# Kernel optimization log

Measured on AMD Instinct MI355X. Metric: run time of the kernel, lower is better.

The kernel has to match this reference:

```python
import jax, jax.numpy as jnp
import numpy as np

KH, KW = 3, 3
PAD = (1, 1, 1, 1)  # torch F.pad order: (W_left, W_right, H_top, H_bottom)
STRIDE = 1
B, CIN, COUT, H, W = 4, 32, 32, 128, 128


def setup_inputs() -> dict:
    key = jax.random.key(0)
    k1, k2, k3, k4 = jax.random.split(key, 4)
    f = jax.random.normal(k1, (B, CIN, H, W), jnp.float32)
    # orientation field components (cos/sin of a random angle field)
    theta = jax.random.uniform(k2, (B, CIN, H, W), jnp.float32, 0.0, 2.0 * np.pi)
    r0 = jnp.cos(theta)
    r1 = jnp.sin(theta)
    # learned conv weight (nn.Conv2d default uniform init, no bias)
    fan_in = CIN * KH * KW
    bound = 1.0 / np.sqrt(fan_in)
    w = jax.random.uniform(k3, (COUT, CIN, KH, KW), jnp.float32, -bound, bound)
    # frozen wr: (randn * pi * 100) / a with a = 100  ->  randn * pi
    wr = jax.random.normal(k4, (COUT, CIN, KH, KW), jnp.float32) * np.pi
    return {"f": f, "r0": r0, "r1": r1, "w": w, "wr": wr}


def _rot90(w):
    # torch: w.permute(0,1,2,4,3).flip([4]) on the (kh,kw) dims
    return jnp.flip(jnp.swapaxes(w, -1, -2), -1)


def _conv_single(f, r0, r1, w, wr):
    # f, r0, r1: (B, Cin, Hp, Wp);  w, wr: (Cout, Cin, KH, KW)
    Hp, Wp = f.shape[2], f.shape[3]
    he = Hp - PAD[0] - PAD[1]
    we = Wp - PAD[2] - PAD[3]
    s = STRIDE
    out = None
    for i in range(KH):
        for j in range(KW):
            fw = f[:, :, i:i + he:s, j:j + we:s]    # (B, Cin, h, w)
            r0w = r0[:, :, i:i + he:s, j:j + we:s]
            r1w = r1[:, :, i:i + he:s, j:j + we:s]
            c = jnp.cos(wr[:, :, i, j])[None, :, :, None, None]   # (1, Cout, Cin, 1, 1)
            sn = jnp.sin(wr[:, :, i, j])[None, :, :, None, None]
            # lambda_theta: relu of orientation-projected field, (B, Cout, Cin, h, w)
            lam = jax.nn.relu(c * r0w[:, None] + sn * r1w[:, None])
            term = jnp.einsum('bchw,oc,bochw->bohw', fw, w[:, :, i, j], lam)
            out = term if out is None else out + term
    return out  # (B, Cout, h, w)


def _forward(f, r0, r1, w, wr):
    pl, pr, pt, pb = PAD
    pad = ((0, 0), (0, 0), (pt, pb), (pl, pr))
    fp = jnp.pad(f, pad)
    r0p = jnp.pad(r0, pad)
    r1p = jnp.pad(r1, pad)
    orient = jnp.arange(4, dtype=f.dtype) * jnp.asarray(np.pi / 2, f.dtype)
    outs = []
    wk = w
    for o in range(4):
        if o > 0:
            wk = _rot90(wk)
        outs.append(_conv_single(fp, r0p, r1p, wk, wr + orient[o]))
    stacked = jnp.stack(outs, axis=2)              # (B, Cout, 4, h, w)
    idx = jnp.argmax(stacked, axis=2)              # (B, Cout, h, w)
    out = jnp.take_along_axis(stacked, idx[:, :, None], axis=2)[:, :, 0]
    out_r = orient[idx]                            # winning orientation angle
    return out, jnp.cos(out_r), jnp.sin(out_r)


def reference(f, r0, r1, w, wr):
    return _forward(f, r0, r1, w, wr)
```

## Files before the change

### kernel.cpp

```cpp
#include <hip/hip_runtime.h>


typedef float v2f __attribute__((ext_vector_type(2)));

#define B_    4
#define CIN_  32
#define COUT_ 32
#define H_    128
#define W_    128
#define OUTSZ_ (B_ * COUT_ * H_ * W_)

__global__ __launch_bounds__(256)
void build_wtab(const float* __restrict__ w, const float* __restrict__ wr,
                float* __restrict__ tab)
{
    int idx = blockIdx.x * 256 + threadIdx.x;
    if (idx >= CIN_ * 9 * COUT_) return;
    int oc  = idx & 31;
    int t2  = idx >> 5;
    int tap = t2 % 9;
    int cc  = t2 / 9;
    int i = tap / 3, j = tap - i * 3;
    int base = (oc * CIN_ + cc) * 9;
    float w0 = w[base + i * 3 + j];
    float w1 = w[base + (2 - j) * 3 + i];
    float w2 = w[base + (2 - i) * 3 + (2 - j)];
    float w3 = w[base + j * 3 + (2 - i)];
    float S, C;
    sincosf(wr[base + i * 3 + j], &S, &C);
    float* dst = tab + (size_t)idx * 8;
    dst[0] = C;  dst[1] = S;
    dst[2] = w0; dst[3] = w1;
    dst[4] = w2; dst[5] = w3;
    dst[6] = 0.0f; dst[7] = 0.0f;
}

__global__ __launch_bounds__(512, 4)
void orient_conv_kernel(const float* __restrict__ f,
                        const float* __restrict__ r0,
                        const float* __restrict__ r1,
                        const float* __restrict__ tab,
                        float* __restrict__ out)
{
    __shared__ float sF[612], sR0[612], sR1[612];

    const int tid   = threadIdx.x;
    const int oc    = tid & 31;
    const int pxg   = tid >> 5;
    const int p     = pxg << 1;
    const int bid   = blockIdx.x;
    const int b     = bid >> 8;
    const int rem   = bid & 255;
    const int h     = rem >> 1;
    const int wbase = (rem & 1) << 6;

    int  r_0 = tid / 68, rm0 = tid - r_0 * 68;
    int  c_0 = rm0 >> 1, s_0 = rm0 & 1;
    int  gh0 = h + r_0 - 1, gw0 = wbase + c_0 + (s_0 << 5) - 1;
    bool ok0 = ((unsigned)gh0 < (unsigned)H_) & ((unsigned)gw0 < (unsigned)W_);
    int  go0 = ok0 ? (gh0 * W_ + gw0) : 0;

    int  sl1 = tid + 512;
    bool hv1 = sl1 < 612;
    int  r_1 = sl1 / 68, rm1 = sl1 - r_1 * 68;
    int  c_1 = rm1 >> 1, s_1 = rm1 & 1;
    int  gh1 = h + r_1 - 1, gw1 = wbase + c_1 + (s_1 << 5) - 1;
    bool ok1 = hv1 & ((unsigned)gh1 < (unsigned)H_) & ((unsigned)gw1 < (unsigned)W_);
    int  go1 = ok1 ? (gh1 * W_ + gw1) : 0;

    const int chanBase = b * (CIN_ * H_ * W_);

    v2f acc[2][4];
#pragma unroll
    for (int q = 0; q < 2; ++q)
#pragma unroll
        for (int o = 0; o < 4; ++o) acc[q][o] = (v2f)(0.0f);

    for (int cc = 0; cc < CIN_; ++cc) {
        const int base = chanBase + cc * (H_ * W_);
        sF [tid] = ok0 ? f [base + go0] : 0.0f;
        sR0[tid] = ok0 ? r0[base + go0] : 0.0f;
        sR1[tid] = ok0 ? r1[base + go0] : 0.0f;
        if (hv1) {
            sF [sl1] = ok1 ? f [base + go1] : 0.0f;
            sR0[sl1] = ok1 ? r0[base + go1] : 0.0f;
            sR1[sl1] = ok1 ? r1[base + go1] : 0.0f;
        }
        __syncthreads();

        const float* wcc = tab + (((size_t)cc * 9) << 5) * 8 + oc * 8;

#pragma unroll
        for (int i = 0; i < 3; ++i) {
            const int wi = i * 68 + (p << 1);
            float4 fA  = *reinterpret_cast<const float4*>(&sF [wi]);
            float4 fB  = *reinterpret_cast<const float4*>(&sF [wi + 4]);
            float4 aA  = *reinterpret_cast<const float4*>(&sR0[wi]);
            float4 aB  = *reinterpret_cast<const float4*>(&sR0[wi + 4]);
            float4 bA  = *reinterpret_cast<const float4*>(&sR1[wi]);
            float4 bB  = *reinterpret_cast<const float4*>(&sR1[wi + 4]);
            v2f fP[4]  = {{fA.x, fA.y}, {fA.z, fA.w}, {fB.x, fB.y}, {fB.z, fB.w}};
            v2f r0P[4] = {{aA.x, aA.y}, {aA.z, aA.w}, {aB.x, aB.y}, {aB.z, aB.w}};
            v2f r1P[4] = {{bA.x, bA.y}, {bA.z, bA.w}, {bB.x, bB.y}, {bB.z, bB.w}};
#pragma unroll
            for (int j = 0; j < 3; ++j) {
                const float* wp = wcc + (i * 3 + j) * 256;
                float4 wA = *reinterpret_cast<const float4*>(wp);
                v2f    wB = *reinterpret_cast<const v2f*>(wp + 4);
                v2f Cd  = {wA.x, wA.x}, Sd  = {wA.y, wA.y};
                v2f w0d = {wA.z, wA.z}, w1d = {wA.w, wA.w};
                v2f w2d = {wB.x, wB.x}, w3d = {wB.y, wB.y};
#pragma unroll
                for (int q = 0; q < 2; ++q) {
                    v2f fv  = fP [q + j];
                    v2f r0v = r0P[q + j];
                    v2f r1v = r1P[q + j];
                    v2f u  = __builtin_elementwise_fma(Cd, r0v, Sd * r1v);
                    v2f vv = __builtin_elementwise_fma(Cd, r1v, -(Sd * r0v));
                    v2f g0 = __builtin_elementwise_max(u,  (v2f)(0.0f));
                    v2f g1 = __builtin_elementwise_max(vv, (v2f)(0.0f));
                    v2f g2 = g0 - u;
                    v2f g3 = g1 - vv;
                    acc[q][0] = __builtin_elementwise_fma(fv * g0, w0d, acc[q][0]);
                    acc[q][1] = __builtin_elementwise_fma(fv * g1, w1d, acc[q][1]);
                    acc[q][2] = __builtin_elementwise_fma(fv * g2, w2d, acc[q][2]);
                    acc[q][3] = __builtin_elementwise_fma(fv * g3, w3d, acc[q][3]);
                }
            }
        }
        __syncthreads();
    }

    const float cosv[4] = {1.0f, -4.37113883e-08f, -1.0f, 1.19248806e-08f};
    const float sinv[4] = {0.0f, 1.0f, -8.74227766e-08f, -1.0f};
#pragma unroll
    for (int q = 0; q < 2; ++q) {
#pragma unroll
        for (int k = 0; k < 2; ++k) {
            int wcol = wbase + p + q + (k << 5);
            float a0 = acc[q][0][k], a1 = acc[q][1][k];
            float a2 = acc[q][2][k], a3 = acc[q][3][k];
            float best = a0; int bi = 0;
            if (a1 > best) { best = a1; bi = 1; }
            if (a2 > best) { best = a2; bi = 2; }
            if (a3 > best) { best = a3; bi = 3; }
            size_t o = ((size_t)(b * COUT_ + oc) * H_ + h) * W_ + wcol;
            out[o]              = best;
            out[o + OUTSZ_]     = cosv[bi];
            out[o + 2 * OUTSZ_] = sinv[bi];
        }
    }
}

extern "C" void kernel_launch(void* const* d_in, const int* in_sizes, int n_in,
                              void* d_out, int out_size, void* d_ws, size_t ws_size,
                              hipStream_t stream)
{
    const float* f  = (const float*)d_in[0];
    const float* r0 = (const float*)d_in[1];
    const float* r1 = (const float*)d_in[2];
    const float* w  = (const float*)d_in[3];
    const float* wr = (const float*)d_in[4];
    float* out = (float*)d_out;
    float* tab = (float*)d_ws;

    build_wtab<<<dim3(36), dim3(256), 0, stream>>>(w, wr, tab);
    orient_conv_kernel<<<dim3(B_ * H_ * 2), dim3(512), 0, stream>>>(
        f, r0, r1, tab, out);
}
```

Baseline: 306.1 us.

## Stage eight input channels per barrier with register prefetch and scalar 4-pixel tiles

```diff
diff --git a/kernel.cpp b/kernel.cpp
--- a/kernel.cpp
+++ b/kernel.cpp
@@ -1,13 +1,12 @@
 #include <hip/hip_runtime.h>
 
-
-typedef float v2f __attribute__((ext_vector_type(2)));
 
 #define B_    4
 #define CIN_  32
 #define COUT_ 32
 #define H_    128
 #define W_    128
+#define HW_   (H_ * W_)
 #define OUTSZ_ (B_ * COUT_ * H_ * W_)
 
 __global__ __launch_bounds__(256)
@@ -35,120 +34,145 @@
     dst[6] = 0.0f; dst[7] = 0.0f;
 }
 
-__global__ __launch_bounds__(512, 4)
+#define NC_   8
+#define SLOTS (NC_ * 3 * 68)
+
+__global__ __launch_bounds__(512, 8)
 void orient_conv_kernel(const float* __restrict__ f,
                         const float* __restrict__ r0,
                         const float* __restrict__ r1,
                         const float* __restrict__ tab,
                         float* __restrict__ out)
 {
-    __shared__ float sF[612], sR0[612], sR1[612];
+    __shared__ float sF[SLOTS], sR0[SLOTS], sR1[SLOTS];
 
     const int tid   = threadIdx.x;
     const int oc    = tid & 31;
     const int pxg   = tid >> 5;
-    const int p     = pxg << 1;
+    const int px0   = pxg << 2;
     const int bid   = blockIdx.x;
     const int b     = bid >> 8;
     const int rem   = bid & 255;
     const int h     = rem >> 1;
     const int wbase = (rem & 1) << 6;
 
-    int  r_0 = tid / 68, rm0 = tid - r_0 * 68;
-    int  c_0 = rm0 >> 1, s_0 = rm0 & 1;
-    int  gh0 = h + r_0 - 1, gw0 = wbase + c_0 + (s_0 << 5) - 1;
-    bool ok0 = ((unsigned)gh0 < (unsigned)H_) & ((unsigned)gw0 < (unsigned)W_);
-    int  go0 = ok0 ? (gh0 * W_ + gw0) : 0;
+    int      goff[4];
+    unsigned msk[4];
+#pragma unroll
+    for (int k = 0; k < 4; ++k) {
+        int s = tid + (k << 9);
+        if (s < SLOTS) {
+            int cc_l = s / 204;
+            int r2   = s - cc_l * 204;
+            int row  = r2 / 68;
+            int col  = r2 - row * 68;
+            int gh = h + row - 1;
+            int gw = wbase + col - 1;
+            bool ok = ((unsigned)gh < (unsigned)H_) & ((unsigned)gw < (unsigned)W_);
+            goff[k] = ok ? (cc_l * HW_ + gh * W_ + gw) : 0;
+            msk[k]  = ok ? 0xFFFFFFFFu : 0u;
+        } else { goff[k] = 0; msk[k] = 0u; }
+    }
+    const bool have3 = (tid + 1536) < SLOTS;
+    const int chanBase = b * (CIN_ * HW_);
 
-    int  sl1 = tid + 512;
-    bool hv1 = sl1 < 612;
-    int  r_1 = sl1 / 68, rm1 = sl1 - r_1 * 68;
-    int  c_1 = rm1 >> 1, s_1 = rm1 & 1;
-    int  gh1 = h + r_1 - 1, gw1 = wbase + c_1 + (s_1 << 5) - 1;
-    bool ok1 = hv1 & ((unsigned)gh1 < (unsigned)H_) & ((unsigned)gw1 < (unsigned)W_);
-    int  go1 = ok1 ? (gh1 * W_ + gw1) : 0;
+    float acc[4][4];
+#pragma unroll
+    for (int p = 0; p < 4; ++p)
+#pragma unroll
+        for (int o = 0; o < 4; ++o) acc[p][o] = 0.0f;
 
-    const int chanBase = b * (CIN_ * H_ * W_);
-
-    v2f acc[2][4];
+#pragma unroll 1
+    for (int g = 0; g < CIN_ / NC_; ++g) {
+        const int gb = chanBase + g * (NC_ * HW_);
+        float tF[4], tA[4], tB[4];
 #pragma unroll
-    for (int q = 0; q < 2; ++q)
+        for (int k = 0; k < 3; ++k) {
+            tF[k] = f [gb + goff[k]];
+            tA[k] = r0[gb + goff[k]];
+            tB[k] = r1[gb + goff[k]];
+        }
+        if (have3) {
+            tF[3] = f [gb + goff[3]];
+            tA[3] = r0[gb + goff[3]];
+            tB[3] = r1[gb + goff[3]];
+        }
+        __syncthreads();
 #pragma unroll
-        for (int o = 0; o < 4; ++o) acc[q][o] = (v2f)(0.0f);
-
-    for (int cc = 0; cc < CIN_; ++cc) {
-        const int base = chanBase + cc * (H_ * W_);
-        sF [tid] = ok0 ? f [base + go0] : 0.0f;
-        sR0[tid] = ok0 ? r0[base + go0] : 0.0f;
-        sR1[tid] = ok0 ? r1[base + go0] : 0.0f;
-        if (hv1) {
-            sF [sl1] = ok1 ? f [base + go1] : 0.0f;
-            sR0[sl1] = ok1 ? r0[base + go1] : 0.0f;
-            sR1[sl1] = ok1 ? r1[base + go1] : 0.0f;
+        for (int k = 0; k < 3; ++k) {
+            int s = tid + (k << 9);
+            sF [s] = __uint_as_float(__float_as_uint(tF[k]) & msk[k]);
+            sR0[s] = __uint_as_float(__float_as_uint(tA[k]) & msk[k]);
+            sR1[s] = __uint_as_float(__float_as_uint(tB[k]) & msk[k]);
+        }
+        if (have3) {
+            int s = tid + 1536;
+            sF [s] = __uint_as_float(__float_as_uint(tF[3]) & msk[3]);
+            sR0[s] = __uint_as_float(__float_as_uint(tA[3]) & msk[3]);
+            sR1[s] = __uint_as_float(__float_as_uint(tB[3]) & msk[3]);
         }
         __syncthreads();
 
-        const float* wcc = tab + (((size_t)cc * 9) << 5) * 8 + oc * 8;
-
+#pragma unroll 1
+        for (int cl = 0; cl < NC_; ++cl) {
+            const int cc = g * NC_ + cl;
+            const float* wcc = tab + ((size_t)(cc * 9) * 32 + oc) * 8;
 #pragma unroll
-        for (int i = 0; i < 3; ++i) {
-            const int wi = i * 68 + (p << 1);
-            float4 fA  = *reinterpret_cast<const float4*>(&sF [wi]);
-            float4 fB  = *reinterpret_cast<const float4*>(&sF [wi + 4]);
-            float4 aA  = *reinterpret_cast<const float4*>(&sR0[wi]);
-            float4 aB  = *reinterpret_cast<const float4*>(&sR0[wi + 4]);
-            float4 bA  = *reinterpret_cast<const float4*>(&sR1[wi]);
-            float4 bB  = *reinterpret_cast<const float4*>(&sR1[wi + 4]);
-            v2f fP[4]  = {{fA.x, fA.y}, {fA.z, fA.w}, {fB.x, fB.y}, {fB.z, fB.w}};
-            v2f r0P[4] = {{aA.x, aA.y}, {aA.z, aA.w}, {aB.x, aB.y}, {aB.z, aB.w}};
-            v2f r1P[4] = {{bA.x, bA.y}, {bA.z, bA.w}, {bB.x, bB.y}, {bB.z, bB.w}};
+            for (int i = 0; i < 3; ++i) {
+                const int bi = cl * 204 + i * 68 + px0;
+                float4 F4 = *reinterpret_cast<const float4*>(&sF [bi]);
+                float2 F2 = *reinterpret_cast<const float2*>(&sF [bi + 4]);
+                float4 A4 = *reinterpret_cast<const float4*>(&sR0[bi]);
+                float2 A2 = *reinterpret_cast<const float2*>(&sR0[bi + 4]);
+                float4 B4 = *reinterpret_cast<const float4*>(&sR1[bi]);
+                float2 B2 = *reinterpret_cast<const float2*>(&sR1[bi + 4]);
+                const float fin[6]  = {F4.x, F4.y, F4.z, F4.w, F2.x, F2.y};
+                const float ain[6]  = {A4.x, A4.y, A4.z, A4.w, A2.x, A2.y};
+                const float bin_[6] = {B4.x, B4.y, B4.z, B4.w, B2.x, B2.y};
 #pragma unroll
-            for (int j = 0; j < 3; ++j) {
-                const float* wp = wcc + (i * 3 + j) * 256;
-                float4 wA = *reinterpret_cast<const float4*>(wp);
-                v2f    wB = *reinterpret_cast<const v2f*>(wp + 4);
-                v2f Cd  = {wA.x, wA.x}, Sd  = {wA.y, wA.y};
-                v2f w0d = {wA.z, wA.z}, w1d = {wA.w, wA.w};
-                v2f w2d = {wB.x, wB.x}, w3d = {wB.y, wB.y};
+                for (int j = 0; j < 3; ++j) {
+                    const float* wp = wcc + (i * 3 + j) * 256;
+                    float4 W4 = *reinterpret_cast<const float4*>(wp);
+                    float2 W2 = *reinterpret_cast<const float2*>(wp + 4);
+                    const float C  = W4.x, S  = W4.y;
+                    const float w0 = W4.z, w1 = W4.w;
+                    const float w2 = W2.x, w3 = W2.y;
 #pragma unroll
-                for (int q = 0; q < 2; ++q) {
-                    v2f fv  = fP [q + j];
-                    v2f r0v = r0P[q + j];
-                    v2f r1v = r1P[q + j];
-                    v2f u  = __builtin_elementwise_fma(Cd, r0v, Sd * r1v);
-                    v2f vv = __builtin_elementwise_fma(Cd, r1v, -(Sd * r0v));
-                    v2f g0 = __builtin_elementwise_max(u,  (v2f)(0.0f));
-                    v2f g1 = __builtin_elementwise_max(vv, (v2f)(0.0f));
-                    v2f g2 = g0 - u;
-                    v2f g3 = g1 - vv;
-                    acc[q][0] = __builtin_elementwise_fma(fv * g0, w0d, acc[q][0]);
-                    acc[q][1] = __builtin_elementwise_fma(fv * g1, w1d, acc[q][1]);
-                    acc[q][2] = __builtin_elementwise_fma(fv * g2, w2d, acc[q][2]);
-                    acc[q][3] = __builtin_elementwise_fma(fv * g3, w3d, acc[q][3]);
+                    for (int p = 0; p < 4; ++p) {
+                        const float fv  = fin [p + j];
+                        const float r0v = ain [p + j];
+                        const float r1v = bin_[p + j];
+                        float u  = fmaf(C, r0v, S * r1v);
+                        float vv = fmaf(C, r1v, -(S * r0v));
+                        float g0 = fmaxf(u,  0.0f);
+                        float g1 = fmaxf(vv, 0.0f);
+                        float g2 = g0 - u;
+                        float g3 = g1 - vv;
+                        acc[p][0] = fmaf(fv * g0, w0, acc[p][0]);
+                        acc[p][1] = fmaf(fv * g1, w1, acc[p][1]);
+                        acc[p][2] = fmaf(fv * g2, w2, acc[p][2]);
+                        acc[p][3] = fmaf(fv * g3, w3, acc[p][3]);
+                    }
                 }
             }
         }
-        __syncthreads();
     }
 
     const float cosv[4] = {1.0f, -4.37113883e-08f, -1.0f, 1.19248806e-08f};
     const float sinv[4] = {0.0f, 1.0f, -8.74227766e-08f, -1.0f};
 #pragma unroll
-    for (int q = 0; q < 2; ++q) {
-#pragma unroll
-        for (int k = 0; k < 2; ++k) {
-            int wcol = wbase + p + q + (k << 5);
-            float a0 = acc[q][0][k], a1 = acc[q][1][k];
-            float a2 = acc[q][2][k], a3 = acc[q][3][k];
-            float best = a0; int bi = 0;
-            if (a1 > best) { best = a1; bi = 1; }
-            if (a2 > best) { best = a2; bi = 2; }
-            if (a3 > best) { best = a3; bi = 3; }
-            size_t o = ((size_t)(b * COUT_ + oc) * H_ + h) * W_ + wcol;
-            out[o]              = best;
-            out[o + OUTSZ_]     = cosv[bi];
-            out[o + 2 * OUTSZ_] = sinv[bi];
-        }
+    for (int p = 0; p < 4; ++p) {
+        int wcol = wbase + px0 + p;
+        float a0 = acc[p][0], a1 = acc[p][1];
+        float a2 = acc[p][2], a3 = acc[p][3];
+        float best = a0; int bi = 0;
+        if (a1 > best) { best = a1; bi = 1; }
+        if (a2 > best) { best = a2; bi = 2; }
+        if (a3 > best) { best = a3; bi = 3; }
+        size_t o = ((size_t)(b * COUT_ + oc) * H_ + h) * W_ + wcol;
+        out[o]              = best;
+        out[o + OUTSZ_]     = cosv[bi];
+        out[o + 2 * OUTSZ_] = sinv[bi];
     }
 }
 
```

Measured after the change: 852.8 us. +178.6%, slower.
